# Kernel tuning notes

Measured on AMD Instinct MI355X. Metric: run time of the kernel, lower is better.

## Reference

```python
import jax, jax.numpy as jnp
import numpy as np

B, N, D, H = 4, 2048, 256, 4
NT, ET = 5, 6
HEAD = D // H


def _linear_params(k, fan_in, fan_out):
    # torch nn.Linear default init: U(-1/sqrt(fan_in), 1/sqrt(fan_in)) for W and b
    bound = 1.0 / np.sqrt(fan_in)
    kw, kb = jax.random.split(k)
    W = jax.random.uniform(kw, (fan_in, fan_out), minval=-bound, maxval=bound, dtype=jnp.float32)
    b = jax.random.uniform(kb, (fan_out,), minval=-bound, maxval=bound, dtype=jnp.float32)
    return W, b


def setup_inputs() -> dict:
    key = jax.random.key(0)
    ks = jax.random.split(key, 10)
    Wq, bq = _linear_params(ks[0], D, D)
    Wk, bk = _linear_params(ks[1], D, D)
    Wv, bv = _linear_params(ks[2], D, D)
    Wo, bo = _linear_params(ks[3], D, D)
    return {
        "nodes": jax.random.normal(ks[4], (B, N, D), dtype=jnp.float32),
        "node_types": jax.random.randint(ks[5], (B, N), 0, NT, dtype=jnp.int32),
        "edge_types": jax.random.randint(ks[6], (B, N, N), 0, ET, dtype=jnp.int32),
        "adjacency": jax.random.randint(ks[7], (B, N, N), 0, 2).astype(jnp.float32),
        "node_type_embed": jax.random.normal(ks[8], (NT, D), dtype=jnp.float32),  # nn.Embedding ~ N(0,1)
        "edge_type_embed": jax.random.normal(ks[9], (ET, H), dtype=jnp.float32),
        "Wq": Wq, "bq": bq, "Wk": Wk, "bk": bk, "Wv": Wv, "bv": bv, "Wo": Wo, "bo": bo,
        "ln_g": jnp.ones((D,), jnp.float32),
        "ln_b": jnp.zeros((D,), jnp.float32),
    }


def reference(nodes, node_types, edge_types, adjacency, node_type_embed, edge_type_embed,
              Wq, bq, Wk, bk, Wv, bv, Wo, bo, ln_g, ln_b):
    # add node-type embeddings (residual below uses the typed nodes, as in the torch code)
    x = nodes + node_type_embed[node_types]                      # [B,N,D]

    def split_heads(t):
        return t.reshape(B, N, H, HEAD).transpose(0, 2, 1, 3)    # [B,H,N,HEAD]

    Q = split_heads(x @ Wq + bq)
    K = split_heads(x @ Wk + bk)
    V = split_heads(x @ Wv + bv)

    scores = jnp.einsum('bhnd,bhmd->bhnm', Q, K) / np.sqrt(HEAD).astype(np.float32)

    # edge-type bias: [B,N,N,H] -> [B,H,N,N]
    scores = scores + jnp.transpose(edge_type_embed[edge_types], (0, 3, 1, 2))

    # type-match soft mask: match -> +0.1, mismatch -> -0.05  (== tm*0.15 - 0.05)
    tm = (node_types[:, :, None] == node_types[:, None, :]).astype(jnp.float32)
    scores = scores + (tm * 0.15 - 0.05)[:, None]

    # adjacency hard mask
    scores = scores + ((1.0 - adjacency) * -1e9)[:, None]

    attn = jax.nn.softmax(scores, axis=-1)                        # [B,H,N,N]
    ctx = jnp.einsum('bhnm,bhmd->bhnd', attn, V)
    ctx = ctx.transpose(0, 2, 1, 3).reshape(B, N, D)

    out = ctx @ Wo + bo
    y = x + out
    mu = jnp.mean(y, axis=-1, keepdims=True)
    var = jnp.var(y, axis=-1, keepdims=True)
    y = (y - mu) * jax.lax.rsqrt(var + 1e-5) * ln_g + ln_b
    return y, attn
```

## Files before the change

kernel.cpp:

```cpp
#include <hip/hip_runtime.h>

#define Bsz 4
#define Nn 2048
#define Dd 256
#define Hh 4
#define HD 64
#define NTt 5
#define ETt 6
#define LOG2E 1.4426950408889634f
#define MSUB 24.0f

typedef float f32x4 __attribute__((ext_vector_type(4)));
typedef __bf16 bf16x8 __attribute__((ext_vector_type(8)));
typedef unsigned int u32x4 __attribute__((ext_vector_type(4)));
typedef unsigned short u16;
typedef unsigned char u8;
typedef unsigned int uint;

static __device__ __forceinline__ u16 f2bf(float f) {
  unsigned int u = __builtin_bit_cast(unsigned int, f);
  u = (u + 0x7fffu + ((u >> 16) & 1u)) >> 16;
  return (u16)u;
}

static __device__ __forceinline__ bf16x8 ld8(const u16* p) {
  return __builtin_bit_cast(bf16x8, *(const u32x4*)p);
}

static __device__ __forceinline__ void stage16(const void* g, void* l) {
  __builtin_amdgcn_global_load_lds(
      (const __attribute__((address_space(1))) uint*)g,
      (__attribute__((address_space(3))) uint*)l, 16, 0, 0);
}

#define MFMA16(a, b, c) __builtin_amdgcn_mfma_f32_16x16x32_bf16((a), (b), (c), 0, 0, 0)

#define OFF_X      0u
#define OFF_XBF    8388608u
#define OFF_WQKVT  12582912u
#define OFF_WOT    12976128u
#define OFF_BQKV   13107200u
#define OFF_Q      13110272u
#define OFF_K      17304576u
#define OFF_V      21498880u
#define OFF_VT     25693184u
#define OFF_CTX    29887488u
#define OFF_CODES  34081792u

__global__ void pack_kernel(const float* Wq, const float* Wk, const float* Wv,
                            const float* Wo, const float* bq, const float* bk,
                            const float* bv, u16* wqkvT, u16* woT, float* bqkv) {
  int tid = blockIdx.x * 256 + threadIdx.x;
  if (tid < 196608) {
    int c = tid >> 8, k = tid & 255;
    int which = c >> 8, cc = c & 255;
    const float* W = (which == 0) ? Wq : ((which == 1) ? Wk : Wv);
    wqkvT[tid] = f2bf(W[k * 256 + cc]);
  } else if (tid < 262144) {
    int t2 = tid - 196608;
    int c = t2 >> 8, k = t2 & 255;
    woT[t2] = f2bf(Wo[k * 256 + c]);
  } else if (tid < 262912) {
    int c = tid - 262144;
    int which = c >> 8, cc = c & 255;
    bqkv[c] = (which == 0) ? bq[cc] : ((which == 1) ? bk[cc] : bv[cc]);
  }
}

__global__ void embed_kernel(const float* nodes, const int* node_types,
                             const float* nte, float* xf, u16* xbf) {
  int t = blockIdx.x * 256 + threadIdx.x;
  int flat = t * 4;
  int bn = flat >> 8, d0 = flat & 255;
  int nt = node_types[bn];
  float4 nv = *(const float4*)(nodes + flat);
  float4 ev = *(const float4*)(nte + nt * 256 + d0);
  float4 x4;
  x4.x = nv.x + ev.x; x4.y = nv.y + ev.y; x4.z = nv.z + ev.z; x4.w = nv.w + ev.w;
  *(float4*)(xf + flat) = x4;
  ushort4 xb;
  xb.x = f2bf(x4.x); xb.y = f2bf(x4.y); xb.z = f2bf(x4.z); xb.w = f2bf(x4.w);
  *(ushort4*)(xbf + flat) = xb;
}

__global__ __launch_bounds__(256) void maskpack_kernel(
    const int* node_types, const int* edge_types, const float* adjacency,
    u8* codes) {
  int t = blockIdx.x * 256 + threadIdx.x;
  int lane = t & 63;
  int kt = (t >> 6) & 31;
  int qt = (t >> 11) & 127;
  int b = t >> 18;
  int l15 = lane & 15, l4 = lane >> 4;
  const int* etb = edge_types + (size_t)b * Nn * Nn;
  const float* adjb = adjacency + (size_t)b * Nn * Nn;
  const int* ntb = node_types + b * Nn;
  int qrow[4], ntq[4], kcol[4], ntk[4];
#pragma unroll
  for (int j = 0; j < 4; ++j) {
    qrow[j] = qt * 16 + l4 * 4 + j;
    ntq[j] = ntb[qrow[j]];
  }
#pragma unroll
  for (int ks = 0; ks < 4; ++ks) {
    kcol[ks] = kt * 64 + ks * 16 + l15;
    ntk[ks] = ntb[kcol[ks]];
  }
  unsigned int w[4];
#pragma unroll
  for (int ks = 0; ks < 4; ++ks) {
    unsigned int acc = 0;
#pragma unroll
    for (int j = 0; j < 4; ++j) {
      size_t e = (size_t)qrow[j] * Nn + kcol[ks];
      int et = etb[e];
      float adj = adjb[e];
      int code = et + ((ntq[j] == ntk[ks]) ? 6 : 0) + ((adj != 0.0f) ? 12 : 0);
      acc |= (unsigned int)(code * 4) << (8 * j);
    }
    w[ks] = acc;
  }
  u32x4 out = {w[0], w[1], w[2], w[3]};
  *(u32x4*)(codes + (size_t)t * 16) = out;
}

__global__ __launch_bounds__(256) void qkv_kernel(const u16* xbf, const u16* wqkvT,
                                                  const float* bqkv,
                                                  u16* Qb, u16* Kb, u16* Vb) {
  int cb = blockIdx.x;
  int rb = blockIdx.y;
  int w = threadIdx.x >> 6, lane = threadIdx.x & 63;
  int l15 = lane & 15, l4 = lane >> 4;
  int row0 = rb * 64 + w * 16;
  int col0 = cb * 64;
  const u16* xr = xbf + (size_t)(row0 + l15) * 256;
  f32x4 acc[4];
#pragma unroll
  for (int i = 0; i < 4; ++i) acc[i] = (f32x4){0.f, 0.f, 0.f, 0.f};
#pragma unroll
  for (int kst = 0; kst < 8; ++kst) {
    int k0 = kst * 32 + l4 * 8;
    bf16x8 a = ld8(xr + k0);
#pragma unroll
    for (int cs = 0; cs < 4; ++cs) {
      int col = col0 + cs * 16 + l15;
      bf16x8 bw = ld8(wqkvT + (size_t)col * 256 + k0);
      acc[cs] = MFMA16(a, bw, acc[cs]);
    }
  }
#pragma unroll
  for (int cs = 0; cs < 4; ++cs) {
    int col = col0 + cs * 16 + l15;
    float bias = bqkv[col];
    int which = col >> 8, c = col & 255;
    int h = c >> 6, hd = c & 63;
    u16* dst = (which == 0) ? Qb : ((which == 1) ? Kb : Vb);
#pragma unroll
    for (int j = 0; j < 4; ++j) {
      int row = row0 + l4 * 4 + j;
      int bb = row >> 11, n = row & 2047;
      dst[(size_t)(((bb * Hh + h) * Nn + n)) * HD + hd] = f2bf(acc[cs][j] + bias);
    }
  }
}

__global__ __launch_bounds__(256) void vtrans_kernel(const u16* Vb, u16* Vtb) {
  int bh = blockIdx.y;
  int d = threadIdx.x & 63;
  int nc = threadIdx.x >> 6;
  int n0 = blockIdx.x * 64 + nc * 16;
  const u16* Vp = Vb + (size_t)bh * Nn * HD;
  union { u16 a[16]; u32x4 v[2]; } tmp;
#pragma unroll
  for (int i = 0; i < 16; ++i) tmp.a[i] = Vp[(size_t)(n0 + i) * HD + d];
  u16* dst = Vtb + ((size_t)bh * HD + d) * Nn + n0;
  *(u32x4*)dst = tmp.v[0];
  *(u32x4*)(dst + 8) = tmp.v[1];
}

__global__ __launch_bounds__(256) void attn_kernel(
    const u16* Qb, const u16* Kb, const u16* Vtb, const u8* codes,
    const float* ee_g, float* attn_out, u16* ctx_ws) {
  __shared__ __align__(16) char kls[2][8192];
  __shared__ __align__(16) char vls[2][8192];
  __shared__ __align__(16) char pls[4][2048];

  int bid0 = blockIdx.x;
  int bid = ((bid0 & 7) << 6) | (bid0 >> 3);
  int qt64 = bid & 31;
  int h = (bid >> 5) & 3;
  int b = bid >> 7;
  int w = threadIdx.x >> 6, lane = threadIdx.x & 63;
  int l15 = lane & 15, l4 = lane >> 4;
  int q0 = qt64 * 64 + w * 16;

  float lutv = 0.f;
  {
    int ln = lane;
    int et = ln - 6 * (ln / 6);
    int tm = (ln / 6) & 1;
    int adj = ln / 12;
    if (ln < 24)
      lutv = (ee_g[et * Hh + h] + (tm ? 0.10f : -0.05f)) * LOG2E +
             (adj ? 0.f : -1.442695041e9f) - MSUB;
  }
  int lut_i = __float_as_int(lutv);

  const u16* Qp = Qb + (size_t)((b * Hh + h) * Nn + q0 + l15) * HD;
  bf16x8 aq0 = ld8(Qp + l4 * 8);
  bf16x8 aq1 = ld8(Qp + 32 + l4 * 8);

  int qrow[4];
#pragma unroll
  for (int j = 0; j < 4; ++j) qrow[j] = q0 + l4 * 4 + j;

  const char* Kg = (const char*)(Kb + (size_t)(b * Hh + h) * Nn * HD);
  const char* Vg = (const char*)(Vtb + (size_t)(b * Hh + h) * HD * Nn);
  const u32x4* cp = (const u32x4*)codes + ((size_t)(b * 128 + (q0 >> 4)) * 32) * 64;
  const float SCL = 0.125f * LOG2E;

  int oT0 = w * 2048 + lane * 16;
  int oT1 = oT0 + 1024;
  int ksw0 = oT0 ^ (((oT0 >> 7) & 7) << 4);
  int ksw1 = oT1 ^ (((oT1 >> 7) & 7) << 4);
  const char* VgR0 = Vg + (size_t)(oT0 >> 7) * (Nn * 2) + (ksw0 & 127);
  const char* VgR1 = Vg + (size_t)(oT1 >> 7) * (Nn * 2) + (ksw1 & 127);

  int sw = (l15 & 7) << 4;
  int ra = (l15 * 128 + l4 * 16) ^ sw;

  stage16(Kg + ksw0, (char*)kls + w * 2048);
  stage16(Kg + ksw1, (char*)kls + w * 2048 + 1024);
  u32x4 cw = cp[lane];
  __syncthreads();

  float accl[4] = {0.f, 0.f, 0.f, 0.f};
#pragma unroll 1
  for (int kt = 0; kt < 32; ++kt) {
    int cb = kt & 1, nb = cb ^ 1;
    u32x4 cwn = cw;
    if (kt < 31) {
      const char* Kn = Kg + (size_t)(kt + 1) * 8192;
      stage16(Kn + ksw0, (char*)kls + nb * 8192 + w * 2048);
      stage16(Kn + ksw1, (char*)kls + nb * 8192 + w * 2048 + 1024);
      cwn = cp[(kt + 1) * 64 + lane];
    }
    const char* kcur = (const char*)kls + cb * 8192;
#pragma unroll
    for (int ks = 0; ks < 4; ++ks) {
      bf16x8 k0 = ld8((const u16*)(kcur + ra + ks * 2048));
      bf16x8 k1 = ld8((const u16*)(kcur + (ra ^ 64) + ks * 2048));
      f32x4 acc = (f32x4){0.f, 0.f, 0.f, 0.f};
      acc = MFMA16(aq0, k0, acc);
      acc = MFMA16(aq1, k1, acc);
      unsigned int cword = cw[ks];
#pragma unroll
      for (int j = 0; j < 4; ++j) {
        int c4 = (cword >> (8 * j)) & 0xFF;
        float bias = __int_as_float(__builtin_amdgcn_ds_bpermute(c4, lut_i));
        accl[j] += __builtin_amdgcn_exp2f(acc[j] * SCL + bias);
      }
    }
    __syncthreads();
    cw = cwn;
  }

  float pscale[4], pbias[4];
#pragma unroll
  for (int j = 0; j < 4; ++j) {
    float v = accl[j];
    v += __shfl_xor(v, 1);
    v += __shfl_xor(v, 2);
    v += __shfl_xor(v, 4);
    v += __shfl_xor(v, 8);
    bool z = (v == 0.0f);
    pscale[j] = z ? 0.0f : 1.0f / v;
    pbias[j] = z ? (1.0f / 2048.0f) : 0.0f;
  }

  float* attb = attn_out + (size_t)(b * Hh + h) * Nn * Nn;
  char* pwave = (char*)pls + w * 2048;
  f32x4 ctx[4];
#pragma unroll
  for (int i = 0; i < 4; ++i) ctx[i] = (f32x4){0.f, 0.f, 0.f, 0.f};

  stage16(Kg + ksw0, (char*)kls + w * 2048);
  stage16(Kg + ksw1, (char*)kls + w * 2048 + 1024);
  stage16(VgR0, (char*)vls + w * 2048);
  stage16(VgR1, (char*)vls + w * 2048 + 1024);
  cw = cp[lane];
  __syncthreads();

#pragma unroll 1
  for (int kt = 0; kt < 32; ++kt) {
    int cb = kt & 1, nb = cb ^ 1;
    u32x4 cwn = cw;
    if (kt < 31) {
      const char* Kn = Kg + (size_t)(kt + 1) * 8192;
      stage16(Kn + ksw0, (char*)kls + nb * 8192 + w * 2048);
      stage16(Kn + ksw1, (char*)kls + nb * 8192 + w * 2048 + 1024);
      stage16(VgR0 + (size_t)(kt + 1) * 128, (char*)vls + nb * 8192 + w * 2048);
      stage16(VgR1 + (size_t)(kt + 1) * 128, (char*)vls + nb * 8192 + w * 2048 + 1024);
      cwn = cp[(kt + 1) * 64 + lane];
    }
    const char* kcur = (const char*)kls + cb * 8192;
    const char* vcur = (const char*)vls + cb * 8192;
    int kbase = kt * 64;
#pragma unroll
    for (int ks = 0; ks < 4; ++ks) {
      bf16x8 k0 = ld8((const u16*)(kcur + ra + ks * 2048));
      bf16x8 k1 = ld8((const u16*)(kcur + (ra ^ 64) + ks * 2048));
      f32x4 acc = (f32x4){0.f, 0.f, 0.f, 0.f};
      acc = MFMA16(aq0, k0, acc);
      acc = MFMA16(aq1, k1, acc);
      unsigned int cword = cw[ks];
      int kcol = kbase + ks * 16 + l15;
#pragma unroll
      for (int j = 0; j < 4; ++j) {
        int c4 = (cword >> (8 * j)) & 0xFF;
        float bias = __int_as_float(__builtin_amdgcn_ds_bpermute(c4, lut_i));
        float p = __builtin_amdgcn_exp2f(acc[j] * SCL + bias) * pscale[j] + pbias[j];
        __builtin_nontemporal_store(p, attb + (size_t)qrow[j] * Nn + kcol);
        int ql = l4 * 4 + j, kl = ks * 16 + l15;
        int byteoff = ql * 128 + ((kl * 2) ^ ((ql & 7) << 4));
        *(u16*)(pwave + byteoff) = f2bf(p);
      }
    }
    int x0 = ((l4 * 8) * 2) ^ ((l15 & 7) << 4);
    int x1 = ((32 + l4 * 8) * 2) ^ ((l15 & 7) << 4);
    bf16x8 pa0 = ld8((const u16*)(pwave + l15 * 128 + x0));
    bf16x8 pa1 = ld8((const u16*)(pwave + l15 * 128 + x1));
#pragma unroll
    for (int ds_ = 0; ds_ < 4; ++ds_) {
      bf16x8 v0 = ld8((const u16*)(vcur + ra + ds_ * 2048));
      bf16x8 v1 = ld8((const u16*)(vcur + (ra ^ 64) + ds_ * 2048));
      ctx[ds_] = MFMA16(pa0, v0, ctx[ds_]);
      ctx[ds_] = MFMA16(pa1, v1, ctx[ds_]);
    }
    asm volatile("s_waitcnt vmcnt(16)" ::: "memory");
    __builtin_amdgcn_s_barrier();
    cw = cwn;
  }

#pragma unroll
  for (int ds_ = 0; ds_ < 4; ++ds_) {
    int col = h * 64 + ds_ * 16 + l15;
#pragma unroll
    for (int j = 0; j < 4; ++j)
      ctx_ws[(size_t)(b * Nn + qrow[j]) * Dd + col] = f2bf(ctx[ds_][j]);
  }
}

__global__ __launch_bounds__(256) void outln_kernel(const u16* ctxb, const u16* woT,
                                                    const float* bo, const float* xf,
                                                    const float* ln_g, const float* ln_b,
                                                    float* yout) {
  __shared__ float ytile[32][257];
  __shared__ float muS[32], rvS[32];
  int bm0 = blockIdx.x * 32;
  int w = threadIdx.x >> 6, lane = threadIdx.x & 63;
  int l15 = lane & 15, l4 = lane >> 4;
  f32x4 acc[2][4];
#pragma unroll
  for (int q = 0; q < 2; ++q)
#pragma unroll
    for (int i = 0; i < 4; ++i) acc[q][i] = (f32x4){0.f, 0.f, 0.f, 0.f};
#pragma unroll
  for (int kst = 0; kst < 8; ++kst) {
    int k0 = kst * 32 + l4 * 8;
    bf16x8 a0 = ld8(ctxb + (size_t)(bm0 + l15) * 256 + k0);
    bf16x8 a1 = ld8(ctxb + (size_t)(bm0 + 16 + l15) * 256 + k0);
#pragma unroll
    for (int ds_ = 0; ds_ < 4; ++ds_) {
      bf16x8 bw = ld8(woT + (size_t)(w * 64 + ds_ * 16 + l15) * 256 + k0);
      acc[0][ds_] = MFMA16(a0, bw, acc[0][ds_]);
      acc[1][ds_] = MFMA16(a1, bw, acc[1][ds_]);
    }
  }
#pragma unroll
  for (int qs = 0; qs < 2; ++qs)
#pragma unroll
    for (int ds_ = 0; ds_ < 4; ++ds_) {
      int col = w * 64 + ds_ * 16 + l15;
      float bof = bo[col];
#pragma unroll
      for (int j = 0; j < 4; ++j) {
        int row = qs * 16 + l4 * 4 + j;
        ytile[row][col] = acc[qs][ds_][j] + bof + xf[(size_t)(bm0 + row) * 256 + col];
      }
    }
  __syncthreads();
  int row = threadIdx.x >> 3, seg = threadIdx.x & 7;
  float ps = 0.f, pq = 0.f;
#pragma unroll
  for (int c = 0; c < 32; ++c) {
    float v = ytile[row][seg * 32 + c];
    ps += v; pq += v * v;
  }
  ps += __shfl_xor(ps, 1); pq += __shfl_xor(pq, 1);
  ps += __shfl_xor(ps, 2); pq += __shfl_xor(pq, 2);
  ps += __shfl_xor(ps, 4); pq += __shfl_xor(pq, 4);
  if (seg == 0) {
    float mu = ps * (1.0f / 256.0f);
    muS[row] = mu;
    rvS[row] = rsqrtf(pq * (1.0f / 256.0f) - mu * mu + 1e-5f);
  }
  __syncthreads();
  float mu = muS[row], rv = rvS[row];
  float* yr = yout + (size_t)(bm0 + row) * 256;
#pragma unroll
  for (int c0 = 0; c0 < 32; c0 += 4) {
    int c = seg * 32 + c0;
    float4 o;
    o.x = (ytile[row][c + 0] - mu) * rv * ln_g[c + 0] + ln_b[c + 0];
    o.y = (ytile[row][c + 1] - mu) * rv * ln_g[c + 1] + ln_b[c + 1];
    o.z = (ytile[row][c + 2] - mu) * rv * ln_g[c + 2] + ln_b[c + 2];
    o.w = (ytile[row][c + 3] - mu) * rv * ln_g[c + 3] + ln_b[c + 3];
    *(float4*)(yr + c) = o;
  }
}

extern "C" void kernel_launch(void* const* d_in, const int* in_sizes, int n_in,
                              void* d_out, int out_size, void* d_ws, size_t ws_size,
                              hipStream_t stream) {
  const float* nodes = (const float*)d_in[0];
  const int* node_types = (const int*)d_in[1];
  const int* edge_types = (const int*)d_in[2];
  const float* adjacency = (const float*)d_in[3];
  const float* nte = (const float*)d_in[4];
  const float* ee = (const float*)d_in[5];
  const float* Wq = (const float*)d_in[6];
  const float* bq = (const float*)d_in[7];
  const float* Wk = (const float*)d_in[8];
  const float* bk = (const float*)d_in[9];
  const float* Wv = (const float*)d_in[10];
  const float* bv = (const float*)d_in[11];
  const float* Wo = (const float*)d_in[12];
  const float* bo = (const float*)d_in[13];
  const float* ln_g = (const float*)d_in[14];
  const float* ln_b = (const float*)d_in[15];

  float* y = (float*)d_out;
  float* attn = y + (size_t)Bsz * Nn * Dd;

  char* ws = (char*)d_ws;
  float* xf = (float*)(ws + OFF_X);
  u16* xbf = (u16*)(ws + OFF_XBF);
  u16* wqkvT = (u16*)(ws + OFF_WQKVT);
  u16* woT = (u16*)(ws + OFF_WOT);
  float* bqkv = (float*)(ws + OFF_BQKV);
  u16* Qb = (u16*)(ws + OFF_Q);
  u16* Kb = (u16*)(ws + OFF_K);
  u16* Vb = (u16*)(ws + OFF_V);
  u16* Vtb = (u16*)(ws + OFF_VT);
  u16* ctxb = (u16*)(ws + OFF_CTX);
  u8* codes = (u8*)(ws + OFF_CODES);

  pack_kernel<<<1027, 256, 0, stream>>>(Wq, Wk, Wv, Wo, bq, bk, bv, wqkvT, woT, bqkv);
  embed_kernel<<<2048, 256, 0, stream>>>(nodes, node_types, nte, xf, xbf);
  maskpack_kernel<<<4096, 256, 0, stream>>>(node_types, edge_types, adjacency, codes);
  qkv_kernel<<<dim3(12, 128), 256, 0, stream>>>(xbf, wqkvT, bqkv, Qb, Kb, Vb);
  vtrans_kernel<<<dim3(32, 16), 256, 0, stream>>>(Vb, Vtb);
  attn_kernel<<<512, 256, 0, stream>>>(Qb, Kb, Vtb, codes, ee, attn, ctxb);
  outln_kernel<<<256, 256, 0, stream>>>(ctxb, woT, bo, xf, ln_g, ln_b, y);
}
```

Measured before the change: 209.8 us.

## Transpose score MFMA so each lane owns a query row, vectorize attn stores

Computes S^T by swapping MFMA operands (K as A, Q as B), so each lane holds four consecutive key columns of one query row. This lets attention probabilities be written as 16-byte nontemporal vector stores and lets the mask codes be read with vectorized int4/float4 loads. The softmax scale and log2e are folded into Q in the QKV kernel, and the bias is used as the MFMA accumulator init, which removes the per-element FMA. Barrier waits are tightened with explicit vmcnt/lgkmcnt and sched barriers. Row-sum reduction becomes two shuffles. The risk is that the explicit waitcnt values could be wrong for the new load counts, and Q rounding after scaling changes numerics slightly.

```diff
diff --git a/kernel.cpp b/kernel.cpp
--- a/kernel.cpp
+++ b/kernel.cpp
@@ -9,10 +9,12 @@
 #define ETt 6
 #define LOG2E 1.4426950408889634f
 #define MSUB 24.0f
+#define SCLQ 0.18033688011112042f
 
 typedef float f32x4 __attribute__((ext_vector_type(4)));
 typedef __bf16 bf16x8 __attribute__((ext_vector_type(8)));
 typedef unsigned int u32x4 __attribute__((ext_vector_type(4)));
+typedef short s16x4 __attribute__((ext_vector_type(4)));
 typedef unsigned short u16;
 typedef unsigned char u8;
 typedef unsigned int uint;
@@ -95,32 +97,29 @@
   const int* etb = edge_types + (size_t)b * Nn * Nn;
   const float* adjb = adjacency + (size_t)b * Nn * Nn;
   const int* ntb = node_types + b * Nn;
-  int qrow[4], ntq[4], kcol[4], ntk[4];
-#pragma unroll
-  for (int j = 0; j < 4; ++j) {
-    qrow[j] = qt * 16 + l4 * 4 + j;
-    ntq[j] = ntb[qrow[j]];
-  }
+  int qrow = qt * 16 + l15;
+  int ntq = ntb[qrow];
+  const int* etr = etb + (size_t)qrow * Nn;
+  const float* adr = adjb + (size_t)qrow * Nn;
+  unsigned int wds[4];
 #pragma unroll
   for (int ks = 0; ks < 4; ++ks) {
-    kcol[ks] = kt * 64 + ks * 16 + l15;
-    ntk[ks] = ntb[kcol[ks]];
-  }
-  unsigned int w[4];
-#pragma unroll
-  for (int ks = 0; ks < 4; ++ks) {
+    int k0 = kt * 64 + ks * 16 + l4 * 4;
+    int4 et4 = *(const int4*)(etr + k0);
+    float4 a4 = *(const float4*)(adr + k0);
+    int4 nt4 = *(const int4*)(ntb + k0);
+    int e[4] = {et4.x, et4.y, et4.z, et4.w};
+    int n[4] = {nt4.x, nt4.y, nt4.z, nt4.w};
+    float a[4] = {a4.x, a4.y, a4.z, a4.w};
     unsigned int acc = 0;
 #pragma unroll
     for (int j = 0; j < 4; ++j) {
-      size_t e = (size_t)qrow[j] * Nn + kcol[ks];
-      int et = etb[e];
-      float adj = adjb[e];
-      int code = et + ((ntq[j] == ntk[ks]) ? 6 : 0) + ((adj != 0.0f) ? 12 : 0);
+      int code = e[j] + ((ntq == n[j]) ? 6 : 0) + ((a[j] != 0.0f) ? 12 : 0);
       acc |= (unsigned int)(code * 4) << (8 * j);
     }
-    w[ks] = acc;
-  }
-  u32x4 out = {w[0], w[1], w[2], w[3]};
+    wds[ks] = acc;
+  }
+  u32x4 out = {wds[0], wds[1], wds[2], wds[3]};
   *(u32x4*)(codes + (size_t)t * 16) = out;
 }
 
@@ -154,12 +153,13 @@
     float bias = bqkv[col];
     int which = col >> 8, c = col & 255;
     int h = c >> 6, hd = c & 63;
+    float scale = (which == 0) ? SCLQ : 1.0f;
     u16* dst = (which == 0) ? Qb : ((which == 1) ? Kb : Vb);
 #pragma unroll
     for (int j = 0; j < 4; ++j) {
       int row = row0 + l4 * 4 + j;
       int bb = row >> 11, n = row & 2047;
-      dst[(size_t)(((bb * Hh + h) * Nn + n)) * HD + hd] = f2bf(acc[cs][j] + bias);
+      dst[(size_t)(((bb * Hh + h) * Nn + n)) * HD + hd] = f2bf((acc[cs][j] + bias) * scale);
     }
   }
 }
@@ -207,17 +207,12 @@
   int lut_i = __float_as_int(lutv);
 
   const u16* Qp = Qb + (size_t)((b * Hh + h) * Nn + q0 + l15) * HD;
-  bf16x8 aq0 = ld8(Qp + l4 * 8);
-  bf16x8 aq1 = ld8(Qp + 32 + l4 * 8);
-
-  int qrow[4];
-#pragma unroll
-  for (int j = 0; j < 4; ++j) qrow[j] = q0 + l4 * 4 + j;
+  bf16x8 bq0 = ld8(Qp + l4 * 8);
+  bf16x8 bq1 = ld8(Qp + 32 + l4 * 8);
 
   const char* Kg = (const char*)(Kb + (size_t)(b * Hh + h) * Nn * HD);
   const char* Vg = (const char*)(Vtb + (size_t)(b * Hh + h) * HD * Nn);
   const u32x4* cp = (const u32x4*)codes + ((size_t)(b * 128 + (q0 >> 4)) * 32) * 64;
-  const float SCL = 0.125f * LOG2E;
 
   int oT0 = w * 2048 + lane * 16;
   int oT1 = oT0 + 1024;
@@ -228,13 +223,14 @@
 
   int sw = (l15 & 7) << 4;
   int ra = (l15 * 128 + l4 * 16) ^ sw;
+  int qa = q0 + l15;
 
   stage16(Kg + ksw0, (char*)kls + w * 2048);
   stage16(Kg + ksw1, (char*)kls + w * 2048 + 1024);
   u32x4 cw = cp[lane];
   __syncthreads();
 
-  float accl[4] = {0.f, 0.f, 0.f, 0.f};
+  float accl = 0.f;
 #pragma unroll 1
   for (int kt = 0; kt < 32; ++kt) {
     int cb = kt & 1, nb = cb ^ 1;
@@ -245,41 +241,35 @@
       stage16(Kn + ksw1, (char*)kls + nb * 8192 + w * 2048 + 1024);
       cwn = cp[(kt + 1) * 64 + lane];
     }
+    __builtin_amdgcn_sched_barrier(0);
     const char* kcur = (const char*)kls + cb * 8192;
 #pragma unroll
     for (int ks = 0; ks < 4; ++ks) {
-      bf16x8 k0 = ld8((const u16*)(kcur + ra + ks * 2048));
-      bf16x8 k1 = ld8((const u16*)(kcur + (ra ^ 64) + ks * 2048));
-      f32x4 acc = (f32x4){0.f, 0.f, 0.f, 0.f};
-      acc = MFMA16(aq0, k0, acc);
-      acc = MFMA16(aq1, k1, acc);
       unsigned int cword = cw[ks];
+      f32x4 acc;
 #pragma unroll
       for (int j = 0; j < 4; ++j) {
         int c4 = (cword >> (8 * j)) & 0xFF;
-        float bias = __int_as_float(__builtin_amdgcn_ds_bpermute(c4, lut_i));
-        accl[j] += __builtin_amdgcn_exp2f(acc[j] * SCL + bias);
+        acc[j] = __int_as_float(__builtin_amdgcn_ds_bpermute(c4, lut_i));
       }
-    }
-    __syncthreads();
+      acc = MFMA16(ld8((const u16*)(kcur + ra + ks * 2048)), bq0, acc);
+      acc = MFMA16(ld8((const u16*)(kcur + (ra ^ 64) + ks * 2048)), bq1, acc);
+      accl += (__builtin_amdgcn_exp2f(acc[0]) + __builtin_amdgcn_exp2f(acc[1])) +
+              (__builtin_amdgcn_exp2f(acc[2]) + __builtin_amdgcn_exp2f(acc[3]));
+    }
+    asm volatile("s_waitcnt vmcnt(1) lgkmcnt(0)" ::: "memory");
+    __builtin_amdgcn_s_barrier();
     cw = cwn;
   }
-
-  float pscale[4], pbias[4];
-#pragma unroll
-  for (int j = 0; j < 4; ++j) {
-    float v = accl[j];
-    v += __shfl_xor(v, 1);
-    v += __shfl_xor(v, 2);
-    v += __shfl_xor(v, 4);
-    v += __shfl_xor(v, 8);
-    bool z = (v == 0.0f);
-    pscale[j] = z ? 0.0f : 1.0f / v;
-    pbias[j] = z ? (1.0f / 2048.0f) : 0.0f;
-  }
-
-  float* attb = attn_out + (size_t)(b * Hh + h) * Nn * Nn;
+  accl += __shfl_xor(accl, 16);
+  accl += __shfl_xor(accl, 32);
+  bool zrow = (accl == 0.0f);
+  float pscale = zrow ? 0.0f : 1.0f / accl;
+  float pbias = zrow ? (1.0f / 2048.0f) : 0.0f;
+
+  float* attb = attn_out + (size_t)(b * Hh + h) * Nn * Nn + (size_t)qa * Nn;
   char* pwave = (char*)pls + w * 2048;
+  int pwbase = l15 * 128;
   f32x4 ctx[4];
 #pragma unroll
   for (int i = 0; i < 4; ++i) ctx[i] = (f32x4){0.f, 0.f, 0.f, 0.f};
@@ -303,33 +293,33 @@
       stage16(VgR1 + (size_t)(kt + 1) * 128, (char*)vls + nb * 8192 + w * 2048 + 1024);
       cwn = cp[(kt + 1) * 64 + lane];
     }
+    __builtin_amdgcn_sched_barrier(0);
     const char* kcur = (const char*)kls + cb * 8192;
     const char* vcur = (const char*)vls + cb * 8192;
-    int kbase = kt * 64;
 #pragma unroll
     for (int ks = 0; ks < 4; ++ks) {
-      bf16x8 k0 = ld8((const u16*)(kcur + ra + ks * 2048));
-      bf16x8 k1 = ld8((const u16*)(kcur + (ra ^ 64) + ks * 2048));
-      f32x4 acc = (f32x4){0.f, 0.f, 0.f, 0.f};
-      acc = MFMA16(aq0, k0, acc);
-      acc = MFMA16(aq1, k1, acc);
       unsigned int cword = cw[ks];
-      int kcol = kbase + ks * 16 + l15;
+      f32x4 acc;
 #pragma unroll
       for (int j = 0; j < 4; ++j) {
         int c4 = (cword >> (8 * j)) & 0xFF;
-        float bias = __int_as_float(__builtin_amdgcn_ds_bpermute(c4, lut_i));
-        float p = __builtin_amdgcn_exp2f(acc[j] * SCL + bias) * pscale[j] + pbias[j];
-        __builtin_nontemporal_store(p, attb + (size_t)qrow[j] * Nn + kcol);
-        int ql = l4 * 4 + j, kl = ks * 16 + l15;
-        int byteoff = ql * 128 + ((kl * 2) ^ ((ql & 7) << 4));
-        *(u16*)(pwave + byteoff) = f2bf(p);
+        acc[j] = __int_as_float(__builtin_amdgcn_ds_bpermute(c4, lut_i));
       }
-    }
-    int x0 = ((l4 * 8) * 2) ^ ((l15 & 7) << 4);
-    int x1 = ((32 + l4 * 8) * 2) ^ ((l15 & 7) << 4);
-    bf16x8 pa0 = ld8((const u16*)(pwave + l15 * 128 + x0));
-    bf16x8 pa1 = ld8((const u16*)(pwave + l15 * 128 + x1));
+      acc = MFMA16(ld8((const u16*)(kcur + ra + ks * 2048)), bq0, acc);
+      acc = MFMA16(ld8((const u16*)(kcur + (ra ^ 64) + ks * 2048)), bq1, acc);
+      f32x4 p;
+#pragma unroll
+      for (int j = 0; j < 4; ++j)
+        p[j] = __builtin_amdgcn_exp2f(acc[j]) * pscale + pbias;
+      __builtin_nontemporal_store(p, (f32x4*)(attb + kt * 64 + ks * 16 + l4 * 4));
+      s16x4 pb;
+#pragma unroll
+      for (int j = 0; j < 4; ++j)
+        pb[j] = (short)__builtin_bit_cast(u16, (__bf16)p[j]);
+      *(s16x4*)(pwave + pwbase + ((ks * 32 + l4 * 8) ^ sw)) = pb;
+    }
+    bf16x8 pa0 = ld8((const u16*)(pwave + pwbase + ((l4 * 16) ^ sw)));
+    bf16x8 pa1 = ld8((const u16*)(pwave + pwbase + ((l4 * 16 + 64) ^ sw)));
 #pragma unroll
     for (int ds_ = 0; ds_ < 4; ++ds_) {
       bf16x8 v0 = ld8((const u16*)(vcur + ra + ds_ * 2048));
@@ -337,7 +327,7 @@
       ctx[ds_] = MFMA16(pa0, v0, ctx[ds_]);
       ctx[ds_] = MFMA16(pa1, v1, ctx[ds_]);
     }
-    asm volatile("s_waitcnt vmcnt(16)" ::: "memory");
+    asm volatile("s_waitcnt vmcnt(5) lgkmcnt(0)" ::: "memory");
     __builtin_amdgcn_s_barrier();
     cw = cwn;
   }
@@ -346,8 +336,10 @@
   for (int ds_ = 0; ds_ < 4; ++ds_) {
     int col = h * 64 + ds_ * 16 + l15;
 #pragma unroll
-    for (int j = 0; j < 4; ++j)
-      ctx_ws[(size_t)(b * Nn + qrow[j]) * Dd + col] = f2bf(ctx[ds_][j]);
+    for (int j = 0; j < 4; ++j) {
+      int qrow = q0 + l4 * 4 + j;
+      ctx_ws[(size_t)(b * Nn + qrow) * Dd + col] = f2bf(ctx[ds_][j]);
+    }
   }
 }
 
```

Result: faster. 193.2 us (-8.0%).
